# Kernel optimization log

Measured on AMD Instinct MI355X. Metric: run time of the kernel, lower is better.

## Reference

```python
import jax, jax.numpy as jnp
import numpy as np

B, S, F, K = 64, 1024, 128, 64  # batch, seq(=l), feat(=d), bottleneck k


def setup_inputs() -> dict:
    key = jax.random.key(0)
    ks = jax.random.split(key, 24)
    r = lambda k_, sh, s=0.05: (jax.random.normal(k_, sh, dtype=jnp.float32) * s)
    inp = {
        'f1_norm': jax.random.normal(ks[0], (B, S, F), dtype=jnp.float32),
        'f2_norm': jax.random.normal(ks[1], (B, S, F), dtype=jnp.float32),
        'f3_norm': jax.random.normal(ks[2], (B, S, F), dtype=jnp.float32),
        # AMLP params (Linear(F, 2F))
        'Wi': r(ks[3], (2 * F, F)), 'bi': r(ks[4], (2 * F,)),
        'Wq': r(ks[5], (2 * F, F)), 'bq': r(ks[6], (2 * F,)),
        'Wvp': r(ks[7], (2 * F, F)), 'bvp': r(ks[8], (2 * F,)),
        # affine_{a,v,l}: Linear(l, l, bias=False) -> weight [l, l]
        'Aa': r(ks[9], (S, S)), 'Av': r(ks[10], (S, S)), 'Al': r(ks[11], (S, S)),
        # W_{a,v,t}: Linear(l, k) -> [k, l]
        'Wa': r(ks[12], (K, S)), 'Wv': r(ks[13], (K, S)), 'Wt': r(ks[14], (K, S)),
        # W_c{a,v,t}: Linear(2d, k) -> [k, 2F]
        'Wca': r(ks[15], (K, 2 * F)), 'Wcv': r(ks[16], (K, 2 * F)), 'Wct': r(ks[17], (K, 2 * F)),
        # W_h{a,v,t}: Linear(k, l) -> [l, k]
        'Wha': r(ks[18], (S, K)), 'Whv': r(ks[19], (S, K)), 'Wht': r(ks[20], (S, K)),
    }
    return inp


def _amlp(txt, aud, vis, Wi, bi, Wq, bq, Wvp, bvp):
    f1 = jnp.einsum('bsf,gf->bsg', txt, Wi) + bi  # [B,S,2F]
    f2 = jnp.einsum('bsf,gf->bsg', aud, Wq) + bq
    f3 = jnp.einsum('bsf,gf->bsg', vis, Wvp) + bvp
    n1 = jnp.linalg.norm(f1)
    n2 = jnp.linalg.norm(f2)
    n3 = jnp.linalg.norm(f3)
    # faithful to source: third term is scalar factor3 * norm3 (broadcast)
    exp_out = (n1 / (n1 + n2)) * f1 + (n2 / (n1 + n2)) * f2 + (n3 / (n1 + n2 + n3)) * n3
    b, s, g = exp_out.shape
    z = exp_out.reshape(b, s, g // 2, 2).sum(-1)  # AvgPool1d(2,2) * 2 == pair sum
    # F.normalize default dim=1 (over sequence axis for 3D tensor)
    z = z / jnp.maximum(jnp.linalg.norm(z, axis=1, keepdims=True), 1e-12)
    return z  # [B,S,F]


def reference(f1_norm, f2_norm, f3_norm, Wi, bi, Wq, bq, Wvp, bvp,
              Aa, Av, Al, Wa, Wv, Wt, Wca, Wcv, Wct, Wha, Whv, Wht):
    txt, aud, vis = f1_norm, f2_norm, f3_norm
    G = _amlp(txt, aud, vis, Wi, bi, Wq, bq, Wvp, bvp)  # [B,S,F]

    G_ag = jnp.concatenate([aud, G], axis=-1)  # [B,S,2F]
    G_vg = jnp.concatenate([vis, G], axis=-1)
    G_lg = jnp.concatenate([txt, G], axis=-1)
    scale = np.sqrt(G_ag.shape[-1]).astype(np.float32)  # sqrt(2F); same for all three

    # a_j = affine(G_xg^T); att = x^T @ a_j^T  ==  x^T @ (A @ G_xg)
    AGa = jnp.einsum('ts,bsc->btc', Aa, G_ag)
    C_a = jnp.tanh(jnp.einsum('bsf,bsc->bfc', aud, AGa) / scale)  # [B,F,2F]
    AGv = jnp.einsum('ts,bsc->btc', Av, G_ag)  # NOTE: source bug uses G_ag, not G_vg
    C_v = jnp.tanh(jnp.einsum('bsf,bsc->bfc', vis, AGv) / scale)
    AGl = jnp.einsum('ts,bsc->btc', Al, G_lg)
    C_t = jnp.tanh(jnp.einsum('bsf,bsc->bfc', txt, AGl) / scale)

    H_a = jax.nn.relu(jnp.einsum('bfc,kc->bfk', C_a, Wca) + jnp.einsum('bsf,ks->bfk', aud, Wa))
    H_v = jax.nn.relu(jnp.einsum('bfc,kc->bfk', C_v, Wcv) + jnp.einsum('bsf,ks->bfk', vis, Wv))
    H_t = jax.nn.relu(jnp.einsum('bfc,kc->bfk', C_t, Wct) + jnp.einsum('bsf,ks->bfk', txt, Wt))

    out_a = jnp.einsum('bfk,sk->bsf', H_a, Wha) + aud  # [B,S,F]
    out_v = jnp.einsum('bfk,sk->bsf', H_v, Whv) + vis
    out_t = jnp.einsum('bfk,sk->bsf', H_t, Wht) + txt
    return (out_t, out_a, out_v)
```

## Files before the change

### kernel.cpp

```cpp
#include <hip/hip_runtime.h>
#include <math.h>

constexpr int Bb = 64;
constexpr int Ss = 1024;
constexpr int Ff = 128;
constexpr int G2 = 256;
constexpr int Kk = 64;
constexpr int NE = 1152;

typedef __bf16 bfrag __attribute__((ext_vector_type(8)));
typedef float  facc  __attribute__((ext_vector_type(4)));
typedef short  s8v   __attribute__((ext_vector_type(8)));

__device__ __forceinline__ short f2bfs(float f) {
  union { float f; unsigned u; } v; v.f = f;
  unsigned r = v.u + 0x7FFFu + ((v.u >> 16) & 1u);
  return (short)(r >> 16);
}
__device__ __forceinline__ float bf2fs(short s) {
  union { unsigned u; float f; } v; v.u = ((unsigned)(unsigned short)s) << 16;
  return v.f;
}
__device__ __forceinline__ facc mfma16(bfrag a, bfrag b, facc c) {
  return __builtin_amdgcn_mfma_f32_16x16x32_bf16(a, b, c, 0, 0, 0);
}
__device__ __forceinline__ void gld16(const void* g, void* l) {
  __builtin_amdgcn_global_load_lds(
      (const __attribute__((address_space(1))) void*)g,
      (__attribute__((address_space(3))) void*)l, 16, 0, 0);
}

__global__ void k_transpose(const float* __restrict__ aud, const float* __restrict__ vis,
                            const float* __restrict__ txt, short* __restrict__ xT) {
  __shared__ float tile[64][65];
  int z = blockIdx.z;
  int mod = z >> 6, b = z & 63;
  const float* x = (mod == 0) ? aud : (mod == 1) ? vis : txt;
  int s0 = blockIdx.x * 64, f0 = blockIdx.y * 64;
  int tid = threadIdx.x;
  for (int i = 0; i < 16; ++i) {
    int idx = i * 256 + tid;
    int si = idx >> 6, fi = idx & 63;
    tile[si][fi] = x[((size_t)b * Ss + s0 + si) * Ff + f0 + fi];
  }
  __syncthreads();
  short* dst = xT + ((size_t)mod * Bb + b) * Ff * Ss;
  for (int i = 0; i < 16; ++i) {
    int idx = i * 256 + tid;
    int fi = idx >> 6, si = idx & 63;
    dst[(size_t)(f0 + fi) * Ss + s0 + si] = f2bfs(tile[si][fi]);
  }
}

__global__ void k_build_aextT(const float* __restrict__ Aa, const float* __restrict__ Av,
                              const float* __restrict__ Al, const float* __restrict__ Wa,
                              const float* __restrict__ Wv, const float* __restrict__ Wt,
                              short* __restrict__ aextT) {
  __shared__ float tile[64][65];
  int mod = blockIdx.z;
  const float* A = (mod == 0) ? Aa : (mod == 1) ? Av : Al;
  const float* W = (mod == 0) ? Wa : (mod == 1) ? Wv : Wt;
  short* dst = aextT + (size_t)mod * NE * Ss;
  int n0 = blockIdx.x * 64, t0 = blockIdx.y * 64;
  int tid = threadIdx.x;
  if (n0 < Ss) {
    for (int i = 0; i < 16; ++i) {
      int idx = i * 256 + tid;
      int ti = idx >> 6, nj = idx & 63;
      tile[ti][nj] = A[(size_t)(t0 + ti) * Ss + n0 + nj];
    }
    __syncthreads();
    for (int i = 0; i < 16; ++i) {
      int idx = i * 256 + tid;
      int nj = idx >> 6, ti = idx & 63;
      dst[(size_t)(n0 + nj) * Ss + t0 + ti] = f2bfs(tile[ti][nj]);
    }
  } else if (n0 < Ss + Kk) {
    for (int i = 0; i < 16; ++i) {
      int idx = i * 256 + tid;
      int j = idx >> 6, tt = idx & 63;
      dst[(size_t)(n0 + j) * Ss + t0 + tt] = f2bfs(W[(size_t)(n0 - Ss + j) * Ss + t0 + tt]);
    }
  } else {
    for (int i = 0; i < 16; ++i) {
      int idx = i * 256 + tid;
      int j = idx >> 6, tt = idx & 63;
      dst[(size_t)(n0 + j) * Ss + t0 + tt] = 0;
    }
  }
}

__global__ void k_build_w(const float* __restrict__ Wca, const float* __restrict__ Wcv,
                          const float* __restrict__ Wct, const float* __restrict__ Wha,
                          const float* __restrict__ Whv, const float* __restrict__ Wht,
                          const float* __restrict__ Wi, const float* __restrict__ Wq,
                          const float* __restrict__ Wvp,
                          short* __restrict__ wcb, short* __restrict__ whb,
                          short* __restrict__ wbar) {
  int idx = blockIdx.x * 256 + threadIdx.x;
  const int n1 = 3 * Kk * G2;
  const int n2 = n1 + 3 * Ss * Kk;
  if (idx < n1) {
    int mod = idx / (Kk * G2), r = idx - mod * (Kk * G2);
    const float* W = (mod == 0) ? Wca : (mod == 1) ? Wcv : Wct;
    wcb[idx] = f2bfs(W[r]);
  } else if (idx < n2) {
    int j = idx - n1;
    int mod = j / (Ss * Kk), r = j - mod * (Ss * Kk);
    const float* W = (mod == 0) ? Wha : (mod == 1) ? Whv : Wht;
    whb[j] = f2bfs(W[r]);
  } else {
    int j = idx - n2;
    int mod = j / (G2 * Ff), r = j - mod * (G2 * Ff);
    int n = r >> 7, k = r & 127;
    const float* W = (mod == 0) ? Wi : (mod == 1) ? Wq : Wvp;
    wbar[mod * G2 * Ff + (((k >> 3) * G2 + n) * 8) + (k & 7)] = f2bfs(W[r]);
  }
}

__global__ void __launch_bounds__(256) k_amlp(
    const float* __restrict__ txt, const float* __restrict__ aud, const float* __restrict__ vis,
    const float* __restrict__ bi, const float* __restrict__ bq, const float* __restrict__ bvp,
    const short* __restrict__ wbar,
    short* __restrict__ p1, short* __restrict__ p2, float* __restrict__ sumsq) {
  int mod = blockIdx.y;
  const float* x    = (mod == 0) ? txt : (mod == 1) ? aud : vis;
  const float* bias = (mod == 0) ? bi  : (mod == 1) ? bq  : bvp;
  const short* wbm  = wbar + mod * G2 * Ff;
  short* pout = (mod == 0) ? p1 : (mod == 1) ? p2 : nullptr;

  __shared__ short wlds[G2 * Ff];
  __shared__ float wred[4];
  int tid = threadIdx.x, lane = tid & 63, wave = tid >> 6;
  int quad = lane >> 4, nl = lane & 15;
  for (int i = 0; i < 16; ++i) {
    int o = (i * 256 + tid) * 8;
    gld16(wbm + o, wlds + o);
  }
  __syncthreads();

  float bia[16];
  for (int t = 0; t < 16; ++t) bia[t] = bias[t * 16 + nl];

  facc zero = {0.f, 0.f, 0.f, 0.f};
  float sq = 0.f;
  for (int rg = 0; rg < 4; ++rg) {
    int arow = blockIdx.x * 256 + rg * 64 + wave * 16 + nl;
    const float* xrow = x + (size_t)arow * Ff;
    facc acc[16];
    for (int t = 0; t < 16; ++t) acc[t] = zero;
    for (int k0 = 0; k0 < Ff; k0 += 32) {
      float4 a0 = *(const float4*)(xrow + k0 + quad * 8);
      float4 a1 = *(const float4*)(xrow + k0 + quad * 8 + 4);
      bfrag af;
      af[0]=(__bf16)a0.x; af[1]=(__bf16)a0.y; af[2]=(__bf16)a0.z; af[3]=(__bf16)a0.w;
      af[4]=(__bf16)a1.x; af[5]=(__bf16)a1.y; af[6]=(__bf16)a1.z; af[7]=(__bf16)a1.w;
      int chunk = (k0 >> 3) + quad;
      for (int t = 0; t < 16; ++t) {
        bfrag bfr = *(const bfrag*)(wlds + ((size_t)chunk * G2 + t * 16 + nl) * 8);
        acc[t] = mfma16(af, bfr, acc[t]);
      }
    }
    int drow = blockIdx.x * 256 + rg * 64 + wave * 16 + quad * 4;
    for (int t = 0; t < 16; ++t) {
      for (int r = 0; r < 4; ++r) {
        float fv = acc[t][r] + bia[t];
        sq += fv * fv;
        if (pout) {
          float fo = fv + __shfl_xor(fv, 1, 64);
          if ((lane & 1) == 0)
            pout[(size_t)(drow + r) * Ff + t * 8 + (nl >> 1)] = f2bfs(fo);
        }
      }
    }
  }
  for (int off = 32; off > 0; off >>= 1) sq += __shfl_down(sq, off, 64);
  if (lane == 0) wred[wave] = sq;
  __syncthreads();
  if (tid == 0) atomicAdd(&sumsq[mod], wred[0] + wred[1] + wred[2] + wred[3]);
}

__global__ void k_colnorm(const short* __restrict__ p1, const short* __restrict__ p2,
                          const float* __restrict__ sumsq, float* __restrict__ colnsq) {
  float n1 = sqrtf(sumsq[0]), n2 = sqrtf(sumsq[1]), n3 = sqrtf(sumsq[2]);
  float w1 = n1 / (n1 + n2), w2 = n2 / (n1 + n2);
  float tc = 2.f * n3 * n3 / (n1 + n2 + n3);
  int b = blockIdx.x, j = threadIdx.x;
  int s0 = blockIdx.y * 64;
  float a = 0.f;
  for (int s = s0; s < s0 + 64; ++s) {
    size_t off = ((size_t)b * Ss + s) * Ff + j;
    float z = w1 * bf2fs(p1[off]) + w2 * bf2fs(p2[off]) + tc;
    a += z * z;
  }
  atomicAdd(&colnsq[b * Ff + j], a);
}

__global__ void k_gnormT(const short* __restrict__ p1, const short* __restrict__ p2,
                         const float* __restrict__ sumsq, const float* __restrict__ colnsq,
                         short* __restrict__ gT) {
  __shared__ float tile[64][65];
  float n1 = sqrtf(sumsq[0]), n2 = sqrtf(sumsq[1]), n3 = sqrtf(sumsq[2]);
  float w1 = n1 / (n1 + n2), w2 = n2 / (n1 + n2);
  float tc = 2.f * n3 * n3 / (n1 + n2 + n3);
  int b = blockIdx.z, s0 = blockIdx.x * 64, f0 = blockIdx.y * 64;
  int tid = threadIdx.x;
  for (int i = 0; i < 16; ++i) {
    int idx = i * 256 + tid;
    int si = idx >> 6, fi = idx & 63;
    size_t off = ((size_t)b * Ss + s0 + si) * Ff + f0 + fi;
    float z = w1 * bf2fs(p1[off]) + w2 * bf2fs(p2[off]) + tc;
    float cn = fmaxf(sqrtf(colnsq[b * Ff + f0 + fi]), 1e-12f);
    tile[si][fi] = z / cn;
  }
  __syncthreads();
  short* dst = gT + (size_t)b * Ff * Ss;
  for (int i = 0; i < 16; ++i) {
    int idx = i * 256 + tid;
    int fi = idx >> 6, si = idx & 63;
    dst[(size_t)(f0 + fi) * Ss + s0 + si] = f2bfs(tile[si][fi]);
  }
}

__global__ void __launch_bounds__(256) k_mgemm(const short* __restrict__ xT,
                                               const short* __restrict__ aextT,
                                               short* __restrict__ mxext) {
  int mod = blockIdx.z;
  const short* Ap = xT + (size_t)mod * Bb * Ff * Ss;
  const short* Bp = aextT + (size_t)mod * NE * Ss;
  short* Op = mxext + (size_t)mod * Bb * Ff * NE;
  int M0 = blockIdx.x * 128, N0 = blockIdx.y * 128;
  __shared__ short As[128 * 64];
  __shared__ short Bs[128 * 64];
  int tid = threadIdx.x, lane = tid & 63, wave = tid >> 6;
  int quad = lane >> 4, nl = lane & 15;
  int wm = (wave >> 1) * 64, wn = (wave & 1) * 64;
  facc zero = {0.f, 0.f, 0.f, 0.f};
  facc acc[4][4];
  for (int i = 0; i < 4; ++i) for (int j = 0; j < 4; ++j) acc[i][j] = zero;
  for (int k0 = 0; k0 < Ss; k0 += 64) {
    __syncthreads();
#pragma unroll
    for (int i = 0; i < 4; ++i) {
      int idx = i * 256 + tid;
      int r = idx >> 3, cs = ((idx & 7) ^ (r & 7)) * 8;
      gld16(Ap + (size_t)(M0 + r) * Ss + k0 + cs, As + idx * 8);
      gld16(Bp + (size_t)(N0 + r) * Ss + k0 + cs, Bs + idx * 8);
    }
    __syncthreads();
#pragma unroll
    for (int kc = 0; kc < 2; ++kc) {
      bfrag a[4], bfr[4];
      for (int mt = 0; mt < 4; ++mt) {
        int row = wm + mt * 16 + nl;
        a[mt] = *(const bfrag*)(As + row * 64 + (((kc * 4 + quad) ^ (row & 7)) * 8));
      }
      for (int nt = 0; nt < 4; ++nt) {
        int row = wn + nt * 16 + nl;
        bfr[nt] = *(const bfrag*)(Bs + row * 64 + (((kc * 4 + quad) ^ (row & 7)) * 8));
      }
      for (int mt = 0; mt < 4; ++mt)
        for (int nt = 0; nt < 4; ++nt)
          acc[mt][nt] = mfma16(a[mt], bfr[nt], acc[mt][nt]);
    }
  }
  for (int mt = 0; mt < 4; ++mt)
    for (int nt = 0; nt < 4; ++nt)
      for (int r = 0; r < 4; ++r) {
        int row = M0 + wm + mt * 16 + quad * 4 + r;
        int col = N0 + wn + nt * 16 + nl;
        Op[(size_t)row * NE + col] = f2bfs(acc[mt][nt][r]);
      }
}

__global__ void __launch_bounds__(512) k_chgemm(const short* __restrict__ mxext,
                                                const short* __restrict__ xT,
                                                const short* __restrict__ gT,
                                                const short* __restrict__ wcb,
                                                short* __restrict__ h) {
  int b = blockIdx.x, mod = blockIdx.y;
  const short* Ap = mxext + ((size_t)mod * Bb + b) * Ff * NE;
  const short* xTb = xT + (size_t)((mod == 2) ? 2 : 0) * Bb * Ff * Ss + (size_t)b * Ff * Ss;
  const short* gTb = gT + (size_t)b * Ff * Ss;
  const short* Wp = wcb + (size_t)mod * Kk * G2;
  short* Hp = h + ((size_t)mod * Bb + b) * Ff * Kk;

  __shared__ short smem[128 * 272];
  short* As = smem;
  short* Bs = smem + 128 * 64;

  int tid = threadIdx.x, lane = tid & 63, wave = tid >> 6;
  int quad = lane >> 4, nl = lane & 15;
  int wm = (wave >> 2) * 64, wn = (wave & 3) * 64;
  facc zero = {0.f, 0.f, 0.f, 0.f};
  facc acc[4][4];
  for (int i = 0; i < 4; ++i) for (int j = 0; j < 4; ++j) acc[i][j] = zero;
  for (int k0 = 0; k0 < Ss; k0 += 64) {
    __syncthreads();
#pragma unroll
    for (int i = 0; i < 2; ++i) {
      int idx = i * 512 + tid;
      int r = idx >> 3, cs = ((idx & 7) ^ (r & 7)) * 8;
      gld16(Ap + (size_t)r * NE + k0 + cs, As + idx * 8);
    }
#pragma unroll
    for (int i = 0; i < 4; ++i) {
      int idx = i * 512 + tid;
      int r = idx >> 3, cs = ((idx & 7) ^ (r & 7)) * 8;
      const short* src = (r < 128) ? (xTb + (size_t)r * Ss) : (gTb + (size_t)(r - 128) * Ss);
      gld16(src + k0 + cs, Bs + idx * 8);
    }
    __syncthreads();
#pragma unroll
    for (int kc = 0; kc < 2; ++kc) {
      bfrag a[4], bfr[4];
      for (int mt = 0; mt < 4; ++mt) {
        int row = wm + mt * 16 + nl;
        a[mt] = *(const bfrag*)(As + row * 64 + (((kc * 4 + quad) ^ (row & 7)) * 8));
      }
      for (int nt = 0; nt < 4; ++nt) {
        int row = wn + nt * 16 + nl;
        bfr[nt] = *(const bfrag*)(Bs + row * 64 + (((kc * 4 + quad) ^ (row & 7)) * 8));
      }
      for (int mt = 0; mt < 4; ++mt)
        for (int nt = 0; nt < 4; ++nt)
          acc[mt][nt] = mfma16(a[mt], bfr[nt], acc[mt][nt]);
    }
  }
  __syncthreads();
  short* Cs = smem;
  for (int mt = 0; mt < 4; ++mt)
    for (int nt = 0; nt < 4; ++nt)
      for (int r = 0; r < 4; ++r) {
        int row = wm + mt * 16 + quad * 4 + r;
        int col = wn + nt * 16 + nl;
        Cs[row * 272 + col] = f2bfs(tanhf(acc[mt][nt][r] * 0.0625f));
      }
  __syncthreads();
  facc hacc[4];
  for (int nt = 0; nt < 4; ++nt) hacc[nt] = zero;
  for (int k0 = 0; k0 < G2; k0 += 32) {
    bfrag ca = *(const bfrag*)(Cs + (wave * 16 + nl) * 272 + k0 + quad * 8);
    for (int nt = 0; nt < 4; ++nt) {
      bfrag wb = *(const bfrag*)(Wp + (size_t)(nt * 16 + nl) * G2 + k0 + quad * 8);
      hacc[nt] = mfma16(ca, wb, hacc[nt]);
    }
  }
  for (int nt = 0; nt < 4; ++nt)
    for (int r = 0; r < 4; ++r) {
      int row = wave * 16 + quad * 4 + r;
      int col = nt * 16 + nl;
      float v = hacc[nt][r] + bf2fs(Ap[(size_t)row * NE + Ss + col]);
      Hp[(size_t)row * Kk + col] = f2bfs(fmaxf(v, 0.f));
    }
}

__global__ void k_outgemm(const short* __restrict__ whb, const short* __restrict__ h,
                          const float* __restrict__ txt, const float* __restrict__ aud,
                          const float* __restrict__ vis, float* __restrict__ outp) {
  int s0 = blockIdx.x * 128, b = blockIdx.y, mod = blockIdx.z;
  const short* Wp = whb + (size_t)mod * Ss * Kk;
  const short* Hp = h + ((size_t)mod * Bb + b) * Ff * Kk;
  const float* xres = ((mod == 0) ? aud : (mod == 1) ? vis : txt) + (size_t)b * Ss * Ff;
  int slot = (mod == 0) ? 1 : (mod == 1) ? 2 : 0;
  float* Op = outp + ((size_t)slot * Bb + b) * Ss * Ff;
  int tid = threadIdx.x, lane = tid & 63, wave = tid >> 6;
  int quad = lane >> 4, nl = lane & 15;
  int wm = (wave >> 1) * 64, wn = (wave & 1) * 64;
  facc zero = {0.f, 0.f, 0.f, 0.f};
  facc acc[4][4];
  for (int i = 0; i < 4; ++i) for (int j = 0; j < 4; ++j) acc[i][j] = zero;
  for (int k0 = 0; k0 < Kk; k0 += 32) {
    bfrag a[4], bfr[4];
    for (int mt = 0; mt < 4; ++mt)
      a[mt] = *(const bfrag*)(Wp + (size_t)(s0 + wm + mt * 16 + nl) * Kk + k0 + quad * 8);
    for (int nt = 0; nt < 4; ++nt)
      bfr[nt] = *(const bfrag*)(Hp + (size_t)(wn + nt * 16 + nl) * Kk + k0 + quad * 8);
    for (int mt = 0; mt < 4; ++mt)
      for (int nt = 0; nt < 4; ++nt)
        acc[mt][nt] = mfma16(a[mt], bfr[nt], acc[mt][nt]);
  }
  for (int mt = 0; mt < 4; ++mt)
    for (int nt = 0; nt < 4; ++nt)
      for (int r = 0; r < 4; ++r) {
        int srow = s0 + wm + mt * 16 + quad * 4 + r;
        int col = wn + nt * 16 + nl;
        size_t o = (size_t)srow * Ff + col;
        Op[o] = acc[mt][nt][r] + xres[o];
      }
}

extern "C" void kernel_launch(void* const* d_in, const int* in_sizes, int n_in,
                              void* d_out, int out_size, void* d_ws, size_t ws_size,
                              hipStream_t stream) {
  const float* txt = (const float*)d_in[0];
  const float* aud = (const float*)d_in[1];
  const float* vis = (const float*)d_in[2];
  const float* Wi  = (const float*)d_in[3];
  const float* bi  = (const float*)d_in[4];
  const float* Wq  = (const float*)d_in[5];
  const float* bq  = (const float*)d_in[6];
  const float* Wvp = (const float*)d_in[7];
  const float* bvp = (const float*)d_in[8];
  const float* Aa  = (const float*)d_in[9];
  const float* Av  = (const float*)d_in[10];
  const float* Al  = (const float*)d_in[11];
  const float* Wa  = (const float*)d_in[12];
  const float* Wv  = (const float*)d_in[13];
  const float* Wt  = (const float*)d_in[14];
  const float* Wca = (const float*)d_in[15];
  const float* Wcv = (const float*)d_in[16];
  const float* Wct = (const float*)d_in[17];
  const float* Wha = (const float*)d_in[18];
  const float* Whv = (const float*)d_in[19];
  const float* Wht = (const float*)d_in[20];

  char* w = (char*)d_ws;
  float* sumsq  = (float*)w;
  float* colnsq = (float*)(w + 256);
  size_t off = 65536;
  short* xT    = (short*)(w + off); off += (size_t)3 * Bb * Ff * Ss * 2;
  short* aextT = (short*)(w + off); off += (size_t)3 * NE * Ss * 2;
  short* gT    = (short*)(w + off); off += (size_t)Bb * Ff * Ss * 2;
  short* mx    = (short*)(w + off);
  short* p1    = mx;
  short* p2    = mx + (size_t)Bb * Ss * Ff;
  off += (size_t)3 * Bb * Ff * NE * 2;
  short* h     = (short*)(w + off); off += (size_t)3 * Bb * Ff * Kk * 2;
  short* wcb   = (short*)(w + off); off += (size_t)3 * Kk * G2 * 2;
  short* whb   = (short*)(w + off); off += (size_t)3 * Ss * Kk * 2;
  short* wbar  = (short*)(w + off); off += (size_t)3 * G2 * Ff * 2;

  hipMemsetAsync(d_ws, 0, 65536, stream);
  k_transpose<<<dim3(16, 2, 192), 256, 0, stream>>>(aud, vis, txt, xT);
  k_build_aextT<<<dim3(NE / 64, 16, 3), 256, 0, stream>>>(Aa, Av, Al, Wa, Wv, Wt, aextT);
  k_build_w<<<(3 * Kk * G2 + 3 * Ss * Kk + 3 * G2 * Ff) / 256, 256, 0, stream>>>(
      Wca, Wcv, Wct, Wha, Whv, Wht, Wi, Wq, Wvp, wcb, whb, wbar);
  k_amlp<<<dim3(Bb * Ss / 256, 3), 256, 0, stream>>>(txt, aud, vis, bi, bq, bvp,
                                                     wbar, p1, p2, sumsq);
  k_colnorm<<<dim3(Bb, 16), 128, 0, stream>>>(p1, p2, sumsq, colnsq);
  k_gnormT<<<dim3(16, 2, Bb), 256, 0, stream>>>(p1, p2, sumsq, colnsq, gT);
  k_mgemm<<<dim3(Bb * Ff / 128, NE / 128, 3), 256, 0, stream>>>(xT, aextT, mx);
  k_chgemm<<<dim3(Bb, 3), 512, 0, stream>>>(mx, xT, gT, wcb, h);
  k_outgemm<<<dim3(Ss / 128, Bb, 3), 256, 0, stream>>>(whb, h, txt, aud, vis, (float*)d_out);
}
```

Baseline: 467.8 us.

## Keep AMLP weight fragments in registers and split output columns across waves

The AMLP projection kernel stops staging the full 64KB bf16 weight matrix in LDS. Each wave now keeps its 64-column slice of weight fragments in registers, using a new pre-swizzled weight layout, and handles all 256 rows of the block. The activation rows are register double-buffered, with the next 16 rows prefetched while the MFMAs run. Dropping the LDS allocation and adding a launch bound of 3 is meant to raise occupancy and remove LDS reads. In exchange, every wave re-reads the same input rows from global memory or cache, four times as often as before.

Measured after the change: 458.3 us. -2.0%, faster.

```diff
diff --git a/kernel.cpp b/kernel.cpp
--- a/kernel.cpp
+++ b/kernel.cpp
@@ -113,12 +113,14 @@
     int j = idx - n2;
     int mod = j / (G2 * Ff), r = j - mod * (G2 * Ff);
     int n = r >> 7, k = r & 127;
+    int t = n >> 4, nl = n & 15;
+    int c = k >> 5, q = (k >> 3) & 3, e = k & 7;
     const float* W = (mod == 0) ? Wi : (mod == 1) ? Wq : Wvp;
-    wbar[mod * G2 * Ff + (((k >> 3) * G2 + n) * 8) + (k & 7)] = f2bfs(W[r]);
-  }
-}
-
-__global__ void __launch_bounds__(256) k_amlp(
+    wbar[mod * G2 * Ff + (((t * 4 + c) * 64 + q * 16 + nl) * 8) + e] = f2bfs(W[r]);
+  }
+}
+
+__global__ void __launch_bounds__(256, 3) k_amlp(
     const float* __restrict__ txt, const float* __restrict__ aud, const float* __restrict__ vis,
     const float* __restrict__ bi, const float* __restrict__ bq, const float* __restrict__ bvp,
     const short* __restrict__ wbar,
@@ -129,50 +131,75 @@
   const short* wbm  = wbar + mod * G2 * Ff;
   short* pout = (mod == 0) ? p1 : (mod == 1) ? p2 : nullptr;
 
-  __shared__ short wlds[G2 * Ff];
   __shared__ float wred[4];
   int tid = threadIdx.x, lane = tid & 63, wave = tid >> 6;
   int quad = lane >> 4, nl = lane & 15;
-  for (int i = 0; i < 16; ++i) {
-    int o = (i * 256 + tid) * 8;
-    gld16(wbm + o, wlds + o);
-  }
-  __syncthreads();
-
-  float bia[16];
-  for (int t = 0; t < 16; ++t) bia[t] = bias[t * 16 + nl];
-
+
+  bfrag wreg[4][4];
+#pragma unroll
+  for (int tt = 0; tt < 4; ++tt)
+#pragma unroll
+    for (int c = 0; c < 4; ++c)
+      wreg[tt][c] = *(const bfrag*)(wbm + ((((wave * 4 + tt) * 4 + c) * 64 + lane) * 8));
+
+  float bia[4];
+#pragma unroll
+  for (int tt = 0; tt < 4; ++tt) bia[tt] = bias[wave * 64 + tt * 16 + nl];
+
+  const float* xblk = x + (size_t)(blockIdx.x * 256) * Ff;
   facc zero = {0.f, 0.f, 0.f, 0.f};
   float sq = 0.f;
-  for (int rg = 0; rg < 4; ++rg) {
-    int arow = blockIdx.x * 256 + rg * 64 + wave * 16 + nl;
-    const float* xrow = x + (size_t)arow * Ff;
-    facc acc[16];
-    for (int t = 0; t < 16; ++t) acc[t] = zero;
-    for (int k0 = 0; k0 < Ff; k0 += 32) {
-      float4 a0 = *(const float4*)(xrow + k0 + quad * 8);
-      float4 a1 = *(const float4*)(xrow + k0 + quad * 8 + 4);
-      bfrag af;
-      af[0]=(__bf16)a0.x; af[1]=(__bf16)a0.y; af[2]=(__bf16)a0.z; af[3]=(__bf16)a0.w;
-      af[4]=(__bf16)a1.x; af[5]=(__bf16)a1.y; af[6]=(__bf16)a1.z; af[7]=(__bf16)a1.w;
-      int chunk = (k0 >> 3) + quad;
-      for (int t = 0; t < 16; ++t) {
-        bfrag bfr = *(const bfrag*)(wlds + ((size_t)chunk * G2 + t * 16 + nl) * 8);
-        acc[t] = mfma16(af, bfr, acc[t]);
-      }
-    }
-    int drow = blockIdx.x * 256 + rg * 64 + wave * 16 + quad * 4;
-    for (int t = 0; t < 16; ++t) {
+
+  float4 buf[8];
+  {
+    const float* xrow = xblk + (size_t)nl * Ff;
+#pragma unroll
+    for (int c = 0; c < 4; ++c) {
+      buf[c * 2]     = *(const float4*)(xrow + c * 32 + quad * 8);
+      buf[c * 2 + 1] = *(const float4*)(xrow + c * 32 + quad * 8 + 4);
+    }
+  }
+
+  for (int g = 0; g < 16; ++g) {
+    bfrag af[4];
+#pragma unroll
+    for (int c = 0; c < 4; ++c) {
+      float4 a0 = buf[c * 2], a1 = buf[c * 2 + 1];
+      af[c][0] = (__bf16)a0.x; af[c][1] = (__bf16)a0.y;
+      af[c][2] = (__bf16)a0.z; af[c][3] = (__bf16)a0.w;
+      af[c][4] = (__bf16)a1.x; af[c][5] = (__bf16)a1.y;
+      af[c][6] = (__bf16)a1.z; af[c][7] = (__bf16)a1.w;
+    }
+    if (g < 15) {
+      const float* xrow = xblk + (size_t)((g + 1) * 16 + nl) * Ff;
+#pragma unroll
+      for (int c = 0; c < 4; ++c) {
+        buf[c * 2]     = *(const float4*)(xrow + c * 32 + quad * 8);
+        buf[c * 2 + 1] = *(const float4*)(xrow + c * 32 + quad * 8 + 4);
+      }
+    }
+    facc acc[4];
+#pragma unroll
+    for (int tt = 0; tt < 4; ++tt) acc[tt] = zero;
+#pragma unroll
+    for (int c = 0; c < 4; ++c)
+#pragma unroll
+      for (int tt = 0; tt < 4; ++tt)
+        acc[tt] = mfma16(af[c], wreg[tt][c], acc[tt]);
+
+    int drow = blockIdx.x * 256 + g * 16 + quad * 4;
+#pragma unroll
+    for (int tt = 0; tt < 4; ++tt)
+#pragma unroll
       for (int r = 0; r < 4; ++r) {
-        float fv = acc[t][r] + bia[t];
+        float fv = acc[tt][r] + bia[tt];
         sq += fv * fv;
         if (pout) {
           float fo = fv + __shfl_xor(fv, 1, 64);
           if ((lane & 1) == 0)
-            pout[(size_t)(drow + r) * Ff + t * 8 + (nl >> 1)] = f2bfs(fo);
+            pout[(size_t)(drow + r) * Ff + wave * 32 + tt * 8 + (nl >> 1)] = f2bfs(fo);
         }
       }
-    }
   }
   for (int off = 32; off > 0; off >>= 1) sq += __shfl_down(sq, off, 64);
   if (lane == 0) wred[wave] = sq;
```
